# Kernel tuning notes

Hardware: AMD Instinct MI355X
Metric: run time of the kernel (lower is better)

The kernel has to match this reference:

```python
import jax, jax.numpy as jnp
import numpy as np

T, B, N, L = 1024, 2, 10000, 30   # frames, batch(=2, hardcoded in original), vocab, glosses/sample
S = 2 * L + 1                      # blank-interleaved (CTC-extended) label length


def setup_inputs() -> dict:
    key = jax.random.key(0)
    k1, k2 = jax.random.split(key)
    logits = jax.random.normal(k1, (T, B, N), dtype=jnp.float32)
    label = jax.random.randint(k2, (B * L,), 1, N, dtype=jnp.int32)  # real glosses are >=1 (0 is blank)
    logits_len = jnp.full((B,), T, dtype=jnp.int32)
    label_len = jnp.full((B,), L, dtype=jnp.int32)
    return {"logits": logits, "logits_len": logits_len, "label": label, "label_len": label_len}


def _extend(lab):
    # [l1, l2, ...] -> [0, l1, 0, l2, ..., 0]  (blank-interleaved), shape (S,)
    return jnp.zeros((S,), lab.dtype).at[1::2].set(lab)


def _reach_fwd(ext):
    # map_forward[j, i] > 0  <=>  state j reachable from start at time i (CTC forward lattice).
    pad2 = jnp.full((2,), -1, ext.dtype)
    allow2 = (ext != 0) & (ext != jnp.concatenate([pad2, ext[:-2]]))  # skip-2 allowed
    init = jnp.zeros((S,), bool).at[0].set(True).at[1].set(True)

    def step(c, _):
        s1 = jnp.concatenate([jnp.zeros((1,), bool), c[:-1]])
        s2 = jnp.concatenate([jnp.zeros((2,), bool), c[:-2]]) & allow2
        n = c | s1 | s2
        return n, n

    _, outs = jax.lax.scan(step, init, None, length=T - 1)
    return jnp.concatenate([init[None], outs], axis=0)  # (T, S)


def _reach_bwd(ext):
    # map_backward[j, i] > 0  <=>  end reachable from state j at time i.
    pad2 = jnp.full((2,), -1, ext.dtype)
    allow2 = (ext != 0) & (ext != jnp.concatenate([ext[2:], pad2]))
    init = jnp.zeros((S,), bool).at[S - 1].set(True).at[S - 2].set(True)

    def step(c, _):
        s1 = jnp.concatenate([c[1:], jnp.zeros((1,), bool)])
        s2 = jnp.concatenate([c[2:], jnp.zeros((2,), bool)]) & allow2
        n = c | s1 | s2
        return n, n

    _, outs = jax.lax.scan(step, init, None, length=T - 1)
    return jnp.concatenate([outs[::-1], init[None]], axis=0)  # (T, S), time 0..T-1


def _forward(logits, label):
    labels = label.reshape(B, L)
    ext = jax.vmap(_extend)(labels)            # (B, S)
    rf = jax.vmap(_reach_fwd)(ext)             # (B, T, S)
    rb = jax.vmap(_reach_bwd)(ext)             # (B, T, S)
    sel = (rf & rb).astype(logits.dtype)       # map_final != 0 on the lattice

    def per_sample(logit, e, s):
        # mask[t, v] = any lattice state j with ext[j] == v active at time t
        mask = jnp.zeros((T, N), logit.dtype).at[:, e].max(s) > 0
        # original builds final_label as a detached numpy copy of logit at masked entries
        target = jax.lax.stop_gradient(jnp.where(mask, logit, jnp.zeros((), logit.dtype)))
        return jnp.sum((logit - target) ** 2)  # nn.MSELoss(reduction='sum')

    losses = jax.vmap(per_sample)(jnp.transpose(logits, (1, 0, 2)), ext, sel)
    return jnp.mean(losses)  # (loss1 + loss2) / 2


def reference(logits, logits_len, label, label_len):
    # logits_len / label_len are fixed to full lengths (T, L) so shapes stay static.
    return _forward(logits, label)
```

## Files before the change

kernel.cpp:

```cpp
#include <hip/hip_runtime.h>
#include <stdint.h>

typedef unsigned long long u64;

static constexpr int T = 1024;
static constexpr int B = 2;
static constexpr int N = 10000;
static constexpr int L = 30;
static constexpr int S = 2 * L + 1;

static constexpr int SUM_BLK  = 1792;
static constexpr int CORR_BLK = 256;
static constexpr int NBLK     = SUM_BLK + CORR_BLK;

static constexpr u64 ALL   = (1ULL << S) - 1;
static constexpr u64 EVENM = 0x5555555555555555ULL & ((1ULL << S) - 1);

__device__ __forceinline__ float block_reduce(float s) {
    for (int off = 32; off; off >>= 1) s += __shfl_down(s, off, 64);
    __shared__ float tmp[8];
    int lane = threadIdx.x & 63, w = threadIdx.x >> 6;
    int nw = blockDim.x >> 6;
    if (lane == 0) tmp[w] = s;
    __syncthreads();
    float t = 0.f;
    if (threadIdx.x == 0)
        for (int i = 0; i < nw; ++i) t += tmp[i];
    return t;
}

__device__ __forceinline__ float sq4(float4 v) {
    return v.x * v.x + v.y * v.y + v.z * v.z + v.w * v.w;
}

__global__ void k_fused(const float4* __restrict__ x4, const float* __restrict__ x,
                        const int* __restrict__ label, float* __restrict__ partials) {
    float s = 0.f;
    if (blockIdx.x < SUM_BLK) {
        const int n4 = (T * B * N) / 4;
        const int stride = SUM_BLK * 256;
        int i0 = blockIdx.x * 256 + threadIdx.x;
        for (int i = i0; i < n4; i += 4 * stride) {
            int i1 = i + stride, i2 = i + 2 * stride, i3 = i + 3 * stride;
            float4 a = x4[i];
            float4 b = (i1 < n4) ? x4[i1] : make_float4(0.f, 0.f, 0.f, 0.f);
            float4 c = (i2 < n4) ? x4[i2] : make_float4(0.f, 0.f, 0.f, 0.f);
            float4 d = (i3 < n4) ? x4[i3] : make_float4(0.f, 0.f, 0.f, 0.f);
            s += sq4(a) + sq4(b) + sq4(c) + sq4(d);
        }
    } else {
        __shared__ int labs[B][L];
        __shared__ u64 dups[B][L];
        __shared__ u64 AfS[B], AbS[B];
        int tid = threadIdx.x;
        if (tid < B) {
            int b = tid;
            int lb[L];
            u64 Af = 0, Ab = 0;
            #pragma unroll
            for (int k = 0; k < L; ++k) { lb[k] = label[b * L + k]; labs[b][k] = lb[k]; }
            #pragma unroll
            for (int k = 0; k < L; ++k) {
                u64 bit = 1ULL << (2 * k + 1);
                if (k == 0     || lb[k] != lb[k - 1]) Af |= bit;
                if (k == L - 1 || lb[k] != lb[k + 1]) Ab |= bit;
                u64 d = 0;
                for (int k2 = 0; k2 < k; ++k2)
                    if (lb[k2] == lb[k]) d |= 1ULL << (2 * k2 + 1);
                dups[b][k] = d;
            }
            AfS[b] = Af; AbS[b] = Ab;
        }
        __syncthreads();
        int pair = (blockIdx.x - SUM_BLK) * 8 + (tid >> 5);
        int lane = tid & 31;
        int b = pair >> 10;
        int t = pair & (T - 1);
        u64 m;
        if (t < 64) {
            u64 Af = AfS[b];
            u64 c = 3ULL;
            for (int i = 0; i < t; ++i) c = (c | (c << 1) | ((c << 2) & Af)) & ALL;
            m = c;
        } else if (t >= T - 64) {
            u64 Ab = AbS[b];
            u64 c = (1ULL << (S - 1)) | (1ULL << (S - 2));
            int n = T - 1 - t;
            for (int i = 0; i < n; ++i) c = c | (c >> 1) | ((c >> 2) & Ab);
            m = c;
        } else {
            m = ALL;
        }
        const float* row = x + (size_t)t * (B * N) + (size_t)b * N;
        if (lane < L) {
            u64 bit = 1ULL << (2 * lane + 1);
            if ((m & bit) && !(m & dups[b][lane])) {
                float v = row[labs[b][lane]];
                s -= v * v;
            }
        } else if (lane == L) {
            if (m & EVENM) { float v = row[0]; s -= v * v; }
        }
    }
    float tot = block_reduce(s);
    if (threadIdx.x == 0) partials[blockIdx.x] = tot;
}

__global__ void k_final(const float* __restrict__ partials, float* __restrict__ out) {
    float s = 0.f;
    for (int i = threadIdx.x; i < NBLK; i += 256) s += partials[i];
    float tot = block_reduce(s);
    if (threadIdx.x == 0) out[0] = 0.5f * tot;
}

extern "C" void kernel_launch(void* const* d_in, const int* in_sizes, int n_in,
                              void* d_out, int out_size, void* d_ws, size_t ws_size,
                              hipStream_t stream) {
    const float* logits = (const float*)d_in[0];
    const int*   label  = (const int*)d_in[2];
    float* partials = (float*)d_ws;

    k_fused<<<NBLK, 256, 0, stream>>>((const float4*)logits, logits, label, partials);
    k_final<<<1, 256, 0, stream>>>(partials, (float*)d_out);
}
```

Measured before the change: 120.3 us.

## Give every block an equal contiguous chunk of the square-sum and co-locate correction work

The old kernel split its blocks into separate roles: 1792 blocks did a grid-strided sum of squares over all logits, and 256 further blocks did only the sparse label corrections. Now all 2048 blocks each sum a fixed contiguous chunk of 2500 float4s, with ten loads per thread issued in two batches of five. The first 256 blocks also do the correction work before their chunk. This is meant to balance load across all blocks and raise memory-level parallelism with explicit batched loads, at the cost of the first 256 blocks carrying extra latency from the correction path.

```diff
diff --git a/kernel.cpp b/kernel.cpp
--- a/kernel.cpp
+++ b/kernel.cpp
@@ -9,9 +9,9 @@
 static constexpr int L = 30;
 static constexpr int S = 2 * L + 1;
 
-static constexpr int SUM_BLK  = 1792;
-static constexpr int CORR_BLK = 256;
-static constexpr int NBLK     = SUM_BLK + CORR_BLK;
+static constexpr int NBLK  = 2048;
+static constexpr int CHUNK = 2500;
+static constexpr int TAIL  = CHUNK - 9 * 256;
 
 static constexpr u64 ALL   = (1ULL << S) - 1;
 static constexpr u64 EVENM = 0x5555555555555555ULL & ((1ULL << S) - 1);
@@ -36,23 +36,12 @@
 __global__ void k_fused(const float4* __restrict__ x4, const float* __restrict__ x,
                         const int* __restrict__ label, float* __restrict__ partials) {
     float s = 0.f;
-    if (blockIdx.x < SUM_BLK) {
-        const int n4 = (T * B * N) / 4;
-        const int stride = SUM_BLK * 256;
-        int i0 = blockIdx.x * 256 + threadIdx.x;
-        for (int i = i0; i < n4; i += 4 * stride) {
-            int i1 = i + stride, i2 = i + 2 * stride, i3 = i + 3 * stride;
-            float4 a = x4[i];
-            float4 b = (i1 < n4) ? x4[i1] : make_float4(0.f, 0.f, 0.f, 0.f);
-            float4 c = (i2 < n4) ? x4[i2] : make_float4(0.f, 0.f, 0.f, 0.f);
-            float4 d = (i3 < n4) ? x4[i3] : make_float4(0.f, 0.f, 0.f, 0.f);
-            s += sq4(a) + sq4(b) + sq4(c) + sq4(d);
-        }
-    } else {
+    int tid = threadIdx.x;
+
+    if (blockIdx.x < 256) {
         __shared__ int labs[B][L];
         __shared__ u64 dups[B][L];
         __shared__ u64 AfS[B], AbS[B];
-        int tid = threadIdx.x;
         if (tid < B) {
             int b = tid;
             int lb[L];
@@ -72,7 +61,7 @@
             AfS[b] = Af; AbS[b] = Ab;
         }
         __syncthreads();
-        int pair = (blockIdx.x - SUM_BLK) * 8 + (tid >> 5);
+        int pair = blockIdx.x * 8 + (tid >> 5);
         int lane = tid & 31;
         int b = pair >> 10;
         int t = pair & (T - 1);
@@ -102,6 +91,19 @@
             if (m & EVENM) { float v = row[0]; s -= v * v; }
         }
     }
+
+    const float4* p = x4 + (size_t)blockIdx.x * CHUNK + tid;
+    float4 v[5];
+    #pragma unroll
+    for (int j = 0; j < 5; ++j) v[j] = p[j * 256];
+    #pragma unroll
+    for (int j = 0; j < 5; ++j) s += sq4(v[j]);
+    #pragma unroll
+    for (int j = 0; j < 4; ++j) v[j] = p[(5 + j) * 256];
+    v[4] = (tid < TAIL) ? p[9 * 256] : make_float4(0.f, 0.f, 0.f, 0.f);
+    #pragma unroll
+    for (int j = 0; j < 5; ++j) s += sq4(v[j]);
+
     float tot = block_reduce(s);
     if (threadIdx.x == 0) partials[blockIdx.x] = tot;
 }
```

Result: no change. 118.8 us (-1.3%).
